# Optimization experiments

Measured on AMD Instinct MI355X. Metric: run time of the kernel, lower is better.

## Reference

```python
import jax, jax.numpy as jnp
import numpy as np
from jax import lax

B, C, H, W = 16, 1, 1024, 1024
BOUNDARY_WEIGHT = 3.0
# two iterations of a flat 5x5 structuring element == one flat 9x9 window
WIN = 9
PAD = WIN // 2


def setup_inputs() -> dict:
    key = jax.random.key(0)
    k1, k2, k3, k4 = jax.random.split(key, 4)
    logits = jax.random.normal(k1, (B, C, H, W), dtype=jnp.float32)
    # spatially-coherent binary masks (random disks), mimicking car masks
    cy = jax.random.uniform(k2, (B,), minval=0.3 * H, maxval=0.7 * H)
    cx = jax.random.uniform(k3, (B,), minval=0.3 * W, maxval=0.7 * W)
    r = jax.random.uniform(k4, (B,), minval=0.15 * H, maxval=0.4 * H)
    ys = jnp.arange(H, dtype=jnp.float32)
    xs = jnp.arange(W, dtype=jnp.float32)
    d2 = (ys[None, :, None] - cy[:, None, None]) ** 2 + (xs[None, None, :] - cx[:, None, None]) ** 2
    targets = (d2 < (r[:, None, None] ** 2)).astype(jnp.float32)[:, None]  # [B,1,H,W]
    return {"logits": logits, "targets": targets}


def _morph(t, op, init):
    # flat-SE morphology over HxW via reduce_window; cv2 default border is
    # the neutral value for the op, matching init padding.
    return lax.reduce_window(
        t, init, op,
        window_dimensions=(1, 1, WIN, WIN),
        window_strides=(1, 1, 1, 1),
        padding=[(0, 0), (0, 0), (PAD, PAD), (PAD, PAD)],
    )


def reference(logits, targets):
    dilated = _morph(targets, lax.max, -jnp.inf)
    eroded = _morph(targets, lax.min, jnp.inf)
    boundary = dilated - eroded  # 1 on mask boundary band, else 0
    weights = 1.0 + (BOUNDARY_WEIGHT - 1.0) * boundary
    # stable BCE-with-logits: max(x,0) - x*y + log1p(exp(-|x|))
    x, y = logits, targets
    per_elem = jnp.maximum(x, 0.0) - x * y + jax.nn.softplus(-jnp.abs(x))
    return jnp.mean(weights * per_elem)
```

## Files before the change

kernel.cpp:

```cpp
#include <hip/hip_runtime.h>

#define BATCH 16
#define IMG_H 1024
#define IMG_W 1024
#define WORDS 16
#define TY 32
#define SROWS (TY + 8)
#define NT 1024
#define NWAVES (NT / 64)

typedef unsigned long long u64;

__global__ void wbce_zero_kernel(float* out) { out[0] = 0.0f; }

__global__ __launch_bounds__(NT, 2)
void wbce_kernel(const float* __restrict__ logits,
                 const float* __restrict__ targets,
                 float* __restrict__ out)
{
    __shared__ u64 sT [SROWS * WORDS];
    __shared__ u64 sHD[SROWS * WORDS];
    __shared__ u64 sHE[SROWS * WORDS];
    __shared__ u64 sBnd[TY * WORDS];
    __shared__ float sRed[NWAVES];

    const int tid  = threadIdx.x;
    const int lane = tid & 63;
    const int wv   = tid >> 6;
    const int rowBase = blockIdx.x * TY;
    const int b = blockIdx.y;

    const float* tgt = targets + (size_t)b * (IMG_H * IMG_W);
    const float* lg  = logits  + (size_t)b * (IMG_H * IMG_W);

    for (int it = wv; it < SROWS * WORDS; it += NWAVES) {
        int sr = it >> 4;
        int w  = it & 15;
        int gr = rowBase + sr - 4;
        float v = 0.0f;
        if (gr >= 0 && gr < IMG_H) v = tgt[gr * IMG_W + w * 64 + lane];
        u64 m = __ballot(v > 0.5f);
        if (lane == 0) sT[it] = m;
    }
    __syncthreads();

    for (int it = tid; it < SROWS * WORDS; it += NT) {
        int sr = it >> 4;
        int w  = it & 15;
        int gr = rowBase + sr - 4;
        u64 hd, he;
        if (gr < 0 || gr >= IMG_H) {
            hd = 0ULL;
            he = ~0ULL;
        } else {
            u64 C  = sT[it];
            u64 Pd = (w > 0)  ? sT[it - 1] : 0ULL;
            u64 Pe = (w > 0)  ? sT[it - 1] : ~0ULL;
            u64 Nd = (w < 15) ? sT[it + 1] : 0ULL;
            u64 Ne = (w < 15) ? sT[it + 1] : ~0ULL;
            u64 d = C, e = C;
            #pragma unroll
            for (int s = 1; s <= 4; ++s) {
                d |= (C >> s) | (Nd << (64 - s));
                d |= (C << s) | (Pd >> (64 - s));
                e &= (C >> s) | (Ne << (64 - s));
                e &= (C << s) | (Pe >> (64 - s));
            }
            hd = d; he = e;
        }
        sHD[it] = hd;
        sHE[it] = he;
    }
    __syncthreads();

    for (int it = tid; it < TY * WORDS; it += NT) {
        int r = it >> 4;
        int w = it & 15;
        u64 d = 0ULL, e = ~0ULL;
        #pragma unroll
        for (int k = 0; k < 9; ++k) {
            d |= sHD[(r + k) * WORDS + w];
            e &= sHE[(r + k) * WORDS + w];
        }
        sBnd[it] = d & ~e;
    }
    __syncthreads();

    float acc = 0.0f;
    #pragma unroll
    for (int k = 0; k < (TY * IMG_W / 4) / NT; ++k) {
        int it  = tid + k * NT;
        int r   = it >> 8;
        int pos = it & 255;
        int w   = pos >> 4;
        int sh  = (pos & 15) * 4;

        const float4 x4 = *(const float4*)(lg + (size_t)(rowBase + r) * IMG_W + pos * 4);
        unsigned int bb = (unsigned int)(sBnd[r * WORDS + w] >> sh);
        unsigned int tb = (unsigned int)(sT[(r + 4) * WORDS + w] >> sh);

        const float xs[4] = {x4.x, x4.y, x4.z, x4.w};
        #pragma unroll
        for (int j = 0; j < 4; ++j) {
            float x  = xs[j];
            float wg = 1.0f + 2.0f * (float)((bb >> j) & 1u);
            float y  = (float)((tb >> j) & 1u);
            float a  = fabsf(x);
            float t  = __builtin_exp2f(a * -1.44269504088896340736f);
            float sp = __builtin_log2f(1.0f + t) * 0.69314718055994530942f;
            float pe = fmaxf(x, 0.0f) - x * y + sp;
            acc = fmaf(wg, pe, acc);
        }
    }

    #pragma unroll
    for (int off = 32; off > 0; off >>= 1)
        acc += __shfl_down(acc, off, 64);
    if (lane == 0) sRed[wv] = acc;
    __syncthreads();
    if (tid == 0) {
        float s = 0.0f;
        #pragma unroll
        for (int i = 0; i < NWAVES; ++i) s += sRed[i];
        atomicAdd(out, s * (1.0f / 16777216.0f));
    }
}

extern "C" void kernel_launch(void* const* d_in, const int* in_sizes, int n_in,
                              void* d_out, int out_size, void* d_ws, size_t ws_size,
                              hipStream_t stream) {
    const float* logits  = (const float*)d_in[0];
    const float* targets = (const float*)d_in[1];
    float* out = (float*)d_out;

    wbce_zero_kernel<<<dim3(1), dim3(1), 0, stream>>>(out);

    dim3 grid(IMG_H / TY, BATCH);
    dim3 block(NT);
    wbce_kernel<<<grid, block, 0, stream>>>(logits, targets, out);
}
```

Before: 40.93 us.

## Prefetch logits into registers before mask stage and batch target loads

Issues all eight float4 logits loads per thread at kernel start so their latency overlaps the target bitmask construction and morphology stages, pinning them with empty asm to keep the compiler from sinking them. Target loading is batched four words per wave iteration to raise memory-level parallelism. Launch bounds are raised to 8 blocks per CU, which caps registers per thread and may force spills given the 32 held logits values.

```diff
diff --git a/kernel.cpp b/kernel.cpp
--- a/kernel.cpp
+++ b/kernel.cpp
@@ -13,7 +13,7 @@
 
 __global__ void wbce_zero_kernel(float* out) { out[0] = 0.0f; }
 
-__global__ __launch_bounds__(NT, 2)
+__global__ __launch_bounds__(NT, 8)
 void wbce_kernel(const float* __restrict__ logits,
                  const float* __restrict__ targets,
                  float* __restrict__ out)
@@ -33,15 +33,35 @@
     const float* tgt = targets + (size_t)b * (IMG_H * IMG_W);
     const float* lg  = logits  + (size_t)b * (IMG_H * IMG_W);
 
-    for (int it = wv; it < SROWS * WORDS; it += NWAVES) {
-        int sr = it >> 4;
-        int w  = it & 15;
+    float4 x[8];
+    #pragma unroll
+    for (int k = 0; k < 8; ++k) {
+        int it  = tid + k * NT;
+        int r   = it >> 8;
+        int pos = it & 255;
+        x[k] = *(const float4*)(lg + (size_t)(rowBase + r) * IMG_W + pos * 4);
+    }
+
+    for (int it4 = wv * 4; it4 < SROWS * WORDS; it4 += NWAVES * 4) {
+        int sr = it4 >> 4;
         int gr = rowBase + sr - 4;
-        float v = 0.0f;
-        if (gr >= 0 && gr < IMG_H) v = tgt[gr * IMG_W + w * 64 + lane];
-        u64 m = __ballot(v > 0.5f);
-        if (lane == 0) sT[it] = m;
+        float v0 = 0.f, v1 = 0.f, v2 = 0.f, v3 = 0.f;
+        if (gr >= 0 && gr < IMG_H) {
+            const float* rp = tgt + (size_t)gr * IMG_W + ((it4 & 15) * 64) + lane;
+            v0 = rp[0]; v1 = rp[64]; v2 = rp[128]; v3 = rp[192];
+        }
+        u64 m0 = __ballot(v0 > 0.5f);
+        u64 m1 = __ballot(v1 > 0.5f);
+        u64 m2 = __ballot(v2 > 0.5f);
+        u64 m3 = __ballot(v3 > 0.5f);
+        if (lane == 0) {
+            sT[it4]     = m0; sT[it4 + 1] = m1;
+            sT[it4 + 2] = m2; sT[it4 + 3] = m3;
+        }
     }
+    #pragma unroll
+    for (int k = 0; k < 8; ++k)
+        asm volatile("" : "+v"(x[k].x), "+v"(x[k].y), "+v"(x[k].z), "+v"(x[k].w));
     __syncthreads();
 
     for (int it = tid; it < SROWS * WORDS; it += NT) {
@@ -54,15 +74,15 @@
             he = ~0ULL;
         } else {
             u64 C  = sT[it];
-            u64 Pd = (w > 0)  ? sT[it - 1] : 0ULL;
-            u64 Pe = (w > 0)  ? sT[it - 1] : ~0ULL;
-            u64 Nd = (w < 15) ? sT[it + 1] : 0ULL;
-            u64 Ne = (w < 15) ? sT[it + 1] : ~0ULL;
+            u64 P  = (w > 0)  ? sT[it - 1] : 0ULL;
+            u64 N  = (w < 15) ? sT[it + 1] : 0ULL;
+            u64 Pe = (w > 0)  ? P : ~0ULL;
+            u64 Ne = (w < 15) ? N : ~0ULL;
             u64 d = C, e = C;
             #pragma unroll
             for (int s = 1; s <= 4; ++s) {
-                d |= (C >> s) | (Nd << (64 - s));
-                d |= (C << s) | (Pd >> (64 - s));
+                d |= (C >> s) | (N  << (64 - s));
+                d |= (C << s) | (P  >> (64 - s));
                 e &= (C >> s) | (Ne << (64 - s));
                 e &= (C << s) | (Pe >> (64 - s));
             }
@@ -88,27 +108,26 @@
 
     float acc = 0.0f;
     #pragma unroll
-    for (int k = 0; k < (TY * IMG_W / 4) / NT; ++k) {
+    for (int k = 0; k < 8; ++k) {
         int it  = tid + k * NT;
         int r   = it >> 8;
         int pos = it & 255;
         int w   = pos >> 4;
         int sh  = (pos & 15) * 4;
 
-        const float4 x4 = *(const float4*)(lg + (size_t)(rowBase + r) * IMG_W + pos * 4);
         unsigned int bb = (unsigned int)(sBnd[r * WORDS + w] >> sh);
         unsigned int tb = (unsigned int)(sT[(r + 4) * WORDS + w] >> sh);
 
-        const float xs[4] = {x4.x, x4.y, x4.z, x4.w};
+        const float xs[4] = {x[k].x, x[k].y, x[k].z, x[k].w};
         #pragma unroll
         for (int j = 0; j < 4; ++j) {
-            float x  = xs[j];
+            float xv = xs[j];
             float wg = 1.0f + 2.0f * (float)((bb >> j) & 1u);
             float y  = (float)((tb >> j) & 1u);
-            float a  = fabsf(x);
+            float a  = fabsf(xv);
             float t  = __builtin_exp2f(a * -1.44269504088896340736f);
             float sp = __builtin_log2f(1.0f + t) * 0.69314718055994530942f;
-            float pe = fmaxf(x, 0.0f) - x * y + sp;
+            float pe = fmaxf(xv, 0.0f) - xv * y + sp;
             acc = fmaf(wg, pe, acc);
         }
     }
```

After: 42.40 us. 1.04x slower.
